# Performance work log

Measured on AMD Instinct MI355X. Metric: run time of the kernel, lower is better.

The kernel has to match this reference:

```python
import jax, jax.numpy as jnp
import numpy as np

N_NODES = 50000
N_EDGES = 800000
IN_DIM = 256
HID = 128
HEADS = 3
N_CLASSES = 40
NEG_SLOPE = 0.2


def gat_conv(x, W, att_src, att_dst, bias, src, dst, n_nodes):
    # x: [N, F_in]; W: [F_in, H*C]; att_*: [H, C]; bias: [H*C]
    H, C = att_src.shape
    h = (x @ W).reshape(n_nodes, H, C)                       # [N,H,C]
    a_src = jnp.einsum('nhc,hc->nh', h, att_src)             # [N,H]
    a_dst = jnp.einsum('nhc,hc->nh', h, att_dst)             # [N,H]
    alpha = jax.nn.leaky_relu(a_src[src] + a_dst[dst], NEG_SLOPE)  # [E,H]
    # softmax over incoming edges per destination node (stable, segment-based)
    amax = jax.ops.segment_max(alpha, dst, num_segments=n_nodes)   # [N,H]
    amax = jnp.where(jnp.isfinite(amax), amax, 0.0)
    ex = jnp.exp(alpha - amax[dst])                          # [E,H]
    denom = jax.ops.segment_sum(ex, dst, num_segments=n_nodes)     # [N,H]
    attn = ex / (denom[dst] + 1e-16)                         # [E,H]
    msg = h[src] * attn[:, :, None]                          # [E,H,C]
    out = jax.ops.segment_sum(msg, dst, num_segments=n_nodes)      # [N,H,C]
    return out.reshape(n_nodes, H * C) + bias


def setup_inputs() -> dict:
    key = jax.random.key(0)
    ks = jax.random.split(key, 12)
    x = jax.random.normal(ks[0], (N_NODES, IN_DIM), dtype=jnp.float32)
    edge_index = jax.random.randint(ks[1], (2, N_EDGES), 0, N_NODES, dtype=jnp.int64)
    s = 0.05
    HC = HEADS * HID
    return {
        'x': x,
        'edge_index': edge_index,
        'W1': jax.random.normal(ks[2], (IN_DIM, HC), dtype=jnp.float32) * s,
        'att_src1': jax.random.normal(ks[3], (HEADS, HID), dtype=jnp.float32) * s,
        'att_dst1': jax.random.normal(ks[4], (HEADS, HID), dtype=jnp.float32) * s,
        'b1': jnp.zeros((HC,), dtype=jnp.float32),
        'W2': jax.random.normal(ks[5], (HC, HC), dtype=jnp.float32) * s,
        'att_src2': jax.random.normal(ks[6], (HEADS, HID), dtype=jnp.float32) * s,
        'att_dst2': jax.random.normal(ks[7], (HEADS, HID), dtype=jnp.float32) * s,
        'b2': jnp.zeros((HC,), dtype=jnp.float32),
        'outW': jax.random.normal(ks[8], (HC, N_CLASSES), dtype=jnp.float32) * s,
        'outb': jnp.zeros((N_CLASSES,), dtype=jnp.float32),
    }


def reference(x, edge_index, W1, att_src1, att_dst1, b1, W2, att_src2, att_dst2, b2, outW, outb):
    n = x.shape[0]
    # PyG GATConv default: add self loops
    loops = jnp.arange(n, dtype=edge_index.dtype)
    src = jnp.concatenate([edge_index[0], loops])
    dst = jnp.concatenate([edge_index[1], loops])
    h = gat_conv(x, W1, att_src1, att_dst1, b1, src, dst, n)
    h = jax.nn.relu(h)  # dropout=0 -> identity
    h = gat_conv(h, W2, att_src2, att_dst2, b2, src, dst, n)
    h = jax.nn.relu(h)
    return h @ outW + outb
```

## Files before the change

kernel.cpp:

```cpp
#include <hip/hip_runtime.h>
#include <cstdint>
#include <cstddef>

typedef unsigned short u16;
typedef unsigned int   u32;
typedef __attribute__((ext_vector_type(8))) short bf16x8;
typedef __attribute__((ext_vector_type(4))) float f32x4;

#define N_NODES 50000
#define N_EDGES 800000
#define ET (N_EDGES + N_NODES)
#define IN_DIM 256
#define HID 128
#define HEADS 3
#define HC 384
#define NCLS 40
#define CAP 96

__device__ __forceinline__ u16 f2bf(float f) {
    union { float f; u32 u; } x; x.f = f;
    u32 r = x.u + 0x7fffu + ((x.u >> 16) & 1u);
    return (u16)(r >> 16);
}
__device__ __forceinline__ float bf2f(u16 b) {
    union { u32 u; float f; } x; x.u = ((u32)b) << 16; return x.f;
}

__device__ __forceinline__ void gload_lds16(const void* g, void* l) {
    __builtin_amdgcn_global_load_lds((const __attribute__((address_space(1))) void*)g,
                                     (__attribute__((address_space(3))) void*)l, 16, 0, 0);
}

__device__ __forceinline__ float rdlane_f(float v, int l) {
    return __int_as_float(__builtin_amdgcn_readlane(__float_as_int(v), l));
}

__global__ __launch_bounds__(256) void count_scatter(const int* __restrict__ ei,
                                                     int* __restrict__ cnt,
                                                     int* __restrict__ bucket)
{
    int e = blockIdx.x * 256 + threadIdx.x;
    if (e >= ET) return;
    int s, d;
    if (e < N_EDGES) { s = ei[e]; d = ei[N_EDGES + e]; }
    else             { s = e - N_EDGES; d = s; }
    int pos = atomicAdd(&cnt[d], 1);
    if (pos < CAP) bucket[d * CAP + pos] = s;
}

__global__ __launch_bounds__(256) void cvt_bf16(const float* __restrict__ in,
                                                u16* __restrict__ o, int n4)
{
    int i = blockIdx.x * 256 + threadIdx.x;
    if (i >= n4) return;
    float4 v = reinterpret_cast<const float4*>(in)[i];
    ushort4 h = { f2bf(v.x), f2bf(v.y), f2bf(v.z), f2bf(v.w) };
    reinterpret_cast<ushort4*>(o)[i] = h;
}

__global__ __launch_bounds__(256) void split_wt(const float* __restrict__ W,
                                                u16* __restrict__ WtH,
                                                u16* __restrict__ WtL, int K)
{
    int idx = blockIdx.x * 256 + threadIdx.x;
    if (idx >= K * HC) return;
    int k = idx / HC, n = idx - k * HC;
    float v = W[idx];
    u16 h = f2bf(v);
    size_t o = ((size_t)(k >> 3) * HC + n) * 8 + (k & 7);
    WtH[o] = h;
    WtL[o] = f2bf(v - bf2f(h));
}

__global__ __launch_bounds__(256) void split_wo(const float* __restrict__ Wo,
                                                u16* __restrict__ WoH,
                                                u16* __restrict__ WoL)
{
    int idx = blockIdx.x * 256 + threadIdx.x;
    if (idx >= HC * 64) return;
    int k = idx >> 6, n = idx & 63;
    float v = (n < NCLS) ? Wo[k * NCLS + n] : 0.f;
    u16 h = f2bf(v);
    size_t o = ((size_t)(k >> 3) * 64 + n) * 8 + (k & 7);
    WoH[o] = h;
    WoL[o] = f2bf(v - bf2f(h));
}

#define BM 128
#define BN 128
#define BK 32
__global__ __launch_bounds__(256) void gemm_mfma(const u16* __restrict__ A,
                                                 const u16* __restrict__ Bh, const u16* __restrict__ Bl,
                                                 u16* __restrict__ Cb, int M, int K)
{
    __shared__ u16 sA0[BM * BK], sA1[BM * BK];
    const int tid = threadIdx.x;
    const int ln  = tid & 63;
    const int wv  = tid >> 6;
    const int bm  = blockIdx.y * BM;
    const int bn  = blockIdx.x * BN;
    const int wm  = (wv >> 1) * 64;
    const int wn  = (wv & 1) * 64;
    const int kg  = ln >> 4;
    const int lr  = ln & 15;
    const int nK  = K >> 5;

    f32x4 acc[4][4] = {};

    auto stage = [&](u16* dA, int ko) {
#pragma unroll
        for (int rnd = 0; rnd < 2; ++rnd) {
            int c   = rnd * 256 + wv * 64 + ln;
            int row = c & 127;
            int kgp = c >> 7;
            int ldsOff = (rnd * 256 + wv * 64) * 8;
            int ar = bm + row; if (ar >= M) ar = M - 1;
            gload_lds16(A + (size_t)ar * K + ko + kgp * 8, dA + ldsOff);
        }
    };

    auto step = [&](const u16* curA, u16* nxtA, int kt, bool pref) {
        const int ko = kt * BK;
        bf16x8 bhf[4], blf[4];
        size_t bb = ((size_t)((ko >> 3) + kg) * HC + bn + wn + lr) * 8;
#pragma unroll
        for (int ni = 0; ni < 4; ++ni) {
            bhf[ni] = *reinterpret_cast<const bf16x8*>(Bh + bb + ni * 128);
            blf[ni] = *reinterpret_cast<const bf16x8*>(Bl + bb + ni * 128);
        }
        if (pref) stage(nxtA, ko + BK);
#pragma unroll
        for (int mi = 0; mi < 4; ++mi) {
            bf16x8 ah = *reinterpret_cast<const bf16x8*>(curA + (kg * 128 + wm + mi * 16 + lr) * 8);
#pragma unroll
            for (int ni = 0; ni < 4; ++ni) {
                acc[mi][ni] = __builtin_amdgcn_mfma_f32_16x16x32_bf16(ah, bhf[ni], acc[mi][ni], 0, 0, 0);
                acc[mi][ni] = __builtin_amdgcn_mfma_f32_16x16x32_bf16(ah, blf[ni], acc[mi][ni], 0, 0, 0);
            }
        }
    };

    stage(sA0, 0);
    for (int kt = 0; kt < nK; kt += 2) {
        __syncthreads();
        step(sA0, sA1, kt, true);
        __syncthreads();
        step(sA1, sA0, kt + 1, kt + 2 < nK);
    }

#pragma unroll
    for (int mi = 0; mi < 4; ++mi) {
#pragma unroll
        for (int i = 0; i < 4; ++i) {
            int r = bm + wm + mi * 16 + kg * 4 + i;
            if (r < M) {
#pragma unroll
                for (int ni = 0; ni < 4; ++ni) {
                    Cb[(size_t)r * HC + bn + wn + ni * 16 + lr] = f2bf(acc[mi][ni][i]);
                }
            }
        }
    }
}

#define OM 256
__global__ __launch_bounds__(256) void out_mfma(const u16* __restrict__ Ah, const u16* __restrict__ Al,
                                                const u16* __restrict__ WoH, const u16* __restrict__ WoL,
                                                const float* __restrict__ b,
                                                float* __restrict__ out)
{
    __shared__ u16 sAh[OM * BK], sAl[OM * BK];
    const int tid = threadIdx.x;
    const int ln  = tid & 63;
    const int wv  = tid >> 6;
    const int bm  = blockIdx.x * OM;
    const int kg  = ln >> 4;
    const int lr  = ln & 15;

    f32x4 acc[4][4] = {};

    for (int kt = 0; kt < HC / BK; ++kt) {
        const int ko = kt * BK;
        __syncthreads();
#pragma unroll
        for (int rnd = 0; rnd < 4; ++rnd) {
            int c   = rnd * 256 + wv * 64 + ln;
            int row = c & 255;
            int kgp = c >> 8;
            int ldsOff = (rnd * 256 + wv * 64) * 8;
            int ar = bm + row; if (ar >= N_NODES) ar = N_NODES - 1;
            size_t off = (size_t)ar * HC + ko + kgp * 8;
            gload_lds16(Ah + off, sAh + ldsOff);
            gload_lds16(Al + off, sAl + ldsOff);
        }
        __syncthreads();

        bf16x8 bhf[4], blf[4];
        size_t bb = ((size_t)((ko >> 3) + kg) * 64 + lr) * 8;
#pragma unroll
        for (int ni = 0; ni < 4; ++ni) {
            bhf[ni] = *reinterpret_cast<const bf16x8*>(WoH + bb + ni * 128);
            blf[ni] = *reinterpret_cast<const bf16x8*>(WoL + bb + ni * 128);
        }
#pragma unroll
        for (int mi = 0; mi < 4; ++mi) {
            int off = (kg * 256 + wv * 64 + mi * 16 + lr) * 8;
            bf16x8 ah = *reinterpret_cast<const bf16x8*>(sAh + off);
            bf16x8 al = *reinterpret_cast<const bf16x8*>(sAl + off);
#pragma unroll
            for (int ni = 0; ni < 4; ++ni) {
                acc[mi][ni] = __builtin_amdgcn_mfma_f32_16x16x32_bf16(ah, bhf[ni], acc[mi][ni], 0, 0, 0);
                acc[mi][ni] = __builtin_amdgcn_mfma_f32_16x16x32_bf16(al, bhf[ni], acc[mi][ni], 0, 0, 0);
                acc[mi][ni] = __builtin_amdgcn_mfma_f32_16x16x32_bf16(ah, blf[ni], acc[mi][ni], 0, 0, 0);
            }
        }
    }

#pragma unroll
    for (int mi = 0; mi < 4; ++mi) {
#pragma unroll
        for (int i = 0; i < 4; ++i) {
            int r = bm + wv * 64 + mi * 16 + kg * 4 + i;
            if (r < N_NODES) {
#pragma unroll
                for (int ni = 0; ni < 4; ++ni) {
                    int col = ni * 16 + lr;
                    if (col < NCLS)
                        out[(size_t)r * NCLS + col] = acc[mi][ni][i] + b[col];
                }
            }
        }
    }
}

__global__ __launch_bounds__(256) void scores_kernel(const u16* __restrict__ h,
                                                     const float* __restrict__ att_s,
                                                     const float* __restrict__ att_d,
                                                     float* __restrict__ asrc,
                                                     float* __restrict__ adst)
{
    int gid = blockIdx.x * 256 + threadIdx.x;
    int wid = gid >> 6;
    int lane = gid & 63;
    if (wid >= N_NODES * HEADS) return;
    int nd = wid / 3;
    int hd = wid - nd * 3;
    const u16* hp = h + (size_t)nd * HC + hd * HID;
    float v0 = bf2f(hp[lane]), v1 = bf2f(hp[lane + 64]);
    float s = v0 * att_s[hd * HID + lane] + v1 * att_s[hd * HID + lane + 64];
    float d = v0 * att_d[hd * HID + lane] + v1 * att_d[hd * HID + lane + 64];
#pragma unroll
    for (int off = 32; off; off >>= 1) {
        s += __shfl_xor(s, off);
        d += __shfl_xor(d, off);
    }
    if (lane == 0) { asrc[wid] = s; adst[wid] = d; }
}

__device__ __forceinline__ float lrelu(float x) { return x > 0.f ? x : 0.2f * x; }

__global__ __launch_bounds__(256) void aggregate_kernel(const u16* __restrict__ h,
                                                        const float* __restrict__ asrc,
                                                        const float* __restrict__ adst,
                                                        const int* __restrict__ cnt,
                                                        const int* __restrict__ bucket,
                                                        const float* __restrict__ bias,
                                                        u16* __restrict__ hOut,
                                                        u16* __restrict__ lOut)
{
    int wv = threadIdx.x >> 6;
    int lane = threadIdx.x & 63;
    int nd = blockIdx.x * 4 + wv;
    if (nd >= N_NODES) return;
    int deg = cnt[nd];
    if (deg > CAP) deg = CAP;
    const int* eb = bucket + nd * CAP;
    float ad0 = adst[nd * 3 + 0], ad1 = adst[nd * 3 + 1], ad2 = adst[nd * 3 + 2];

    bool vA = lane < deg, vB = lane + 64 < deg;
    int sA = vA ? eb[lane] : 0;
    int sB = vB ? eb[lane + 64] : 0;
    float xA0 = -1e30f, xA1 = -1e30f, xA2 = -1e30f;
    float xB0 = -1e30f, xB1 = -1e30f, xB2 = -1e30f;
    if (vA) {
        const float* ap = asrc + (size_t)sA * 3;
        xA0 = lrelu(ap[0] + ad0); xA1 = lrelu(ap[1] + ad1); xA2 = lrelu(ap[2] + ad2);
    }
    if (vB) {
        const float* ap = asrc + (size_t)sB * 3;
        xB0 = lrelu(ap[0] + ad0); xB1 = lrelu(ap[1] + ad1); xB2 = lrelu(ap[2] + ad2);
    }
    float m0 = fmaxf(xA0, xB0), m1 = fmaxf(xA1, xB1), m2 = fmaxf(xA2, xB2);
#pragma unroll
    for (int off = 32; off; off >>= 1) {
        m0 = fmaxf(m0, __shfl_xor(m0, off));
        m1 = fmaxf(m1, __shfl_xor(m1, off));
        m2 = fmaxf(m2, __shfl_xor(m2, off));
    }
    float eA0 = expf(xA0 - m0), eA1 = expf(xA1 - m1), eA2 = expf(xA2 - m2);
    float eB0 = expf(xB0 - m0), eB1 = expf(xB1 - m1), eB2 = expf(xB2 - m2);
    float t0 = eA0 + eB0, t1 = eA1 + eB1, t2 = eA2 + eB2;
#pragma unroll
    for (int off = 32; off; off >>= 1) {
        t0 += __shfl_xor(t0, off);
        t1 += __shfl_xor(t1, off);
        t2 += __shfl_xor(t2, off);
    }
    float r0 = 1.f / (t0 + 1e-16f);
    float r1 = 1.f / (t1 + 1e-16f);
    float r2 = 1.f / (t2 + 1e-16f);
    float wA0 = eA0 * r0, wA1 = eA1 * r1, wA2 = eA2 * r2;
    float wB0 = eB0 * r0, wB1 = eB1 * r1, wB2 = eB2 * r2;

    float a00 = 0.f, a01 = 0.f, a10 = 0.f, a11 = 0.f, a20 = 0.f, a21 = 0.f;
    int d0 = deg < 64 ? deg : 64;
    for (int j = 0; j < d0; ++j) {
        int   s  = __builtin_amdgcn_readlane(sA, j);
        float w0 = rdlane_f(wA0, j);
        float w1 = rdlane_f(wA1, j);
        float w2 = rdlane_f(wA2, j);
        const u16* hp = h + (size_t)s * HC;
        ushort2 h0 = *reinterpret_cast<const ushort2*>(hp + lane * 2);
        ushort2 h1 = *reinterpret_cast<const ushort2*>(hp + 128 + lane * 2);
        ushort2 h2 = *reinterpret_cast<const ushort2*>(hp + 256 + lane * 2);
        a00 += bf2f(h0.x) * w0; a01 += bf2f(h0.y) * w0;
        a10 += bf2f(h1.x) * w1; a11 += bf2f(h1.y) * w1;
        a20 += bf2f(h2.x) * w2; a21 += bf2f(h2.y) * w2;
    }
    for (int j = 64; j < deg; ++j) {
        int   s  = __builtin_amdgcn_readlane(sB, j - 64);
        float w0 = rdlane_f(wB0, j - 64);
        float w1 = rdlane_f(wB1, j - 64);
        float w2 = rdlane_f(wB2, j - 64);
        const u16* hp = h + (size_t)s * HC;
        ushort2 h0 = *reinterpret_cast<const ushort2*>(hp + lane * 2);
        ushort2 h1 = *reinterpret_cast<const ushort2*>(hp + 128 + lane * 2);
        ushort2 h2 = *reinterpret_cast<const ushort2*>(hp + 256 + lane * 2);
        a00 += bf2f(h0.x) * w0; a01 += bf2f(h0.y) * w0;
        a10 += bf2f(h1.x) * w1; a11 += bf2f(h1.y) * w1;
        a20 += bf2f(h2.x) * w2; a21 += bf2f(h2.y) * w2;
    }

    size_t base = (size_t)nd * HC;
    float o[6];
    int   c[3] = { lane * 2, 128 + lane * 2, 256 + lane * 2 };
    o[0] = a00 + bias[c[0]];     o[1] = a01 + bias[c[0] + 1];
    o[2] = a10 + bias[c[1]];     o[3] = a11 + bias[c[1] + 1];
    o[4] = a20 + bias[c[2]];     o[5] = a21 + bias[c[2] + 1];
#pragma unroll
    for (int k = 0; k < 6; ++k) o[k] = o[k] > 0.f ? o[k] : 0.f;
    if (lOut) {
#pragma unroll
        for (int k = 0; k < 3; ++k) {
            u16 hx = f2bf(o[2 * k]), hy = f2bf(o[2 * k + 1]);
            ushort2 hv = { hx, hy };
            ushort2 lv = { f2bf(o[2 * k] - bf2f(hx)), f2bf(o[2 * k + 1] - bf2f(hy)) };
            *reinterpret_cast<ushort2*>(hOut + base + c[k]) = hv;
            *reinterpret_cast<ushort2*>(lOut + base + c[k]) = lv;
        }
    } else {
#pragma unroll
        for (int k = 0; k < 3; ++k) {
            ushort2 hv = { f2bf(o[2 * k]), f2bf(o[2 * k + 1]) };
            *reinterpret_cast<ushort2*>(hOut + base + c[k]) = hv;
        }
    }
}

extern "C" void kernel_launch(void* const* d_in, const int* in_sizes, int n_in,
                              void* d_out, int out_size, void* d_ws, size_t ws_size,
                              hipStream_t stream)
{
    const float* x    = (const float*)d_in[0];
    const int*   ei   = (const int*)d_in[1];
    const float* W1   = (const float*)d_in[2];
    const float* as1  = (const float*)d_in[3];
    const float* ad1  = (const float*)d_in[4];
    const float* b1   = (const float*)d_in[5];
    const float* W2   = (const float*)d_in[6];
    const float* as2  = (const float*)d_in[7];
    const float* ad2  = (const float*)d_in[8];
    const float* b2   = (const float*)d_in[9];
    const float* outW = (const float*)d_in[10];
    const float* outb = (const float*)d_in[11];
    float* out = (float*)d_out;

    u16*   hB   = (u16*)d_ws;
    u16*   aggH = hB + (size_t)N_NODES * HC;
    u16*   aggL = aggH + (size_t)N_NODES * HC;
    u16*   xB   = aggH;
    char*  tail = (char*)(aggL + (size_t)N_NODES * HC);
    u16* W1tH = (u16*)tail;
    u16* W1tL = W1tH + (size_t)IN_DIM * HC;
    u16* W2tH = W1tL + (size_t)IN_DIM * HC;
    u16* W2tL = W2tH + (size_t)HC * HC;
    u16* WoH  = W2tL + (size_t)HC * HC;
    u16* WoL  = WoH + (size_t)HC * 64;
    float* asrc = (float*)(WoL + (size_t)HC * 64);
    float* adst = asrc + (size_t)N_NODES * HEADS;
    int*   cnt    = (int*)(adst + (size_t)N_NODES * HEADS);
    int*   bucket = cnt + N_NODES;

    hipMemsetAsync(cnt, 0, N_NODES * sizeof(int), stream);
    count_scatter<<<(ET + 255) / 256, 256, 0, stream>>>(ei, cnt, bucket);

    cvt_bf16<<<(N_NODES * IN_DIM / 4 + 255) / 256, 256, 0, stream>>>(x, xB, N_NODES * IN_DIM / 4);
    split_wt<<<(IN_DIM * HC + 255) / 256, 256, 0, stream>>>(W1, W1tH, W1tL, IN_DIM);
    split_wt<<<(HC * HC + 255) / 256, 256, 0, stream>>>(W2, W2tH, W2tL, HC);
    split_wo<<<(HC * 64 + 255) / 256, 256, 0, stream>>>(outW, WoH, WoL);

    dim3 gg(HC / BN, (N_NODES + BM - 1) / BM);
    gemm_mfma<<<gg, 256, 0, stream>>>(xB, W1tH, W1tL, hB, N_NODES, IN_DIM);
    scores_kernel<<<(N_NODES * HEADS + 3) / 4, 256, 0, stream>>>(hB, as1, ad1, asrc, adst);
    aggregate_kernel<<<(N_NODES + 3) / 4, 256, 0, stream>>>(hB, asrc, adst, cnt, bucket, b1,
                                                            aggH, nullptr);
    gemm_mfma<<<gg, 256, 0, stream>>>(aggH, W2tH, W2tL, hB, N_NODES, HC);
    scores_kernel<<<(N_NODES * HEADS + 3) / 4, 256, 0, stream>>>(hB, as2, ad2, asrc, adst);
    aggregate_kernel<<<(N_NODES + 3) / 4, 256, 0, stream>>>(hB, asrc, adst, cnt, bucket, b2,
                                                            aggH, aggL);
    out_mfma<<<(N_NODES + OM - 1) / OM, 256, 0, stream>>>(aggH, aggL, WoH, WoL, outb, out);
}
```

Before: 533.5 us.

## Fuse attention score computation into GEMM epilogue and widen aggregate loads

```diff
diff --git a/kernel.cpp b/kernel.cpp
--- a/kernel.cpp
+++ b/kernel.cpp
@@ -91,9 +91,14 @@
 #define BK 32
 __global__ __launch_bounds__(256) void gemm_mfma(const u16* __restrict__ A,
                                                  const u16* __restrict__ Bh, const u16* __restrict__ Bl,
+                                                 const float* __restrict__ att_s,
+                                                 const float* __restrict__ att_d,
+                                                 float* __restrict__ asrc,
+                                                 float* __restrict__ adst,
                                                  u16* __restrict__ Cb, int M, int K)
 {
     __shared__ u16 sA0[BM * BK], sA1[BM * BK];
+    __shared__ float sS[2][BM], sD[2][BM];
     const int tid = threadIdx.x;
     const int ln  = tid & 63;
     const int wv  = tid >> 6;
@@ -161,6 +166,43 @@
             }
         }
     }
+
+    const int hd = blockIdx.x;
+    float as_[4], ad_[4];
+#pragma unroll
+    for (int ni = 0; ni < 4; ++ni) {
+        int colh = wn + ni * 16 + lr;
+        as_[ni] = att_s[hd * HID + colh];
+        ad_[ni] = att_d[hd * HID + colh];
+    }
+#pragma unroll
+    for (int mi = 0; mi < 4; ++mi) {
+#pragma unroll
+        for (int i = 0; i < 4; ++i) {
+            float ps = acc[mi][0][i] * as_[0] + acc[mi][1][i] * as_[1]
+                     + acc[mi][2][i] * as_[2] + acc[mi][3][i] * as_[3];
+            float pd = acc[mi][0][i] * ad_[0] + acc[mi][1][i] * ad_[1]
+                     + acc[mi][2][i] * ad_[2] + acc[mi][3][i] * ad_[3];
+#pragma unroll
+            for (int off = 1; off < 16; off <<= 1) {
+                ps += __shfl_xor(ps, off);
+                pd += __shfl_xor(pd, off);
+            }
+            if (lr == 0) {
+                int rl = wm + mi * 16 + kg * 4 + i;
+                sS[wv & 1][rl] = ps;
+                sD[wv & 1][rl] = pd;
+            }
+        }
+    }
+    __syncthreads();
+    if (tid < BM) {
+        int r = bm + tid;
+        if (r < M) {
+            asrc[r * 3 + hd] = sS[0][tid] + sS[1][tid];
+            adst[r * 3 + hd] = sD[0][tid] + sD[1][tid];
+        }
+    }
 }
 
 #define OM 256
@@ -233,30 +275,6 @@
     }
 }
 
-__global__ __launch_bounds__(256) void scores_kernel(const u16* __restrict__ h,
-                                                     const float* __restrict__ att_s,
-                                                     const float* __restrict__ att_d,
-                                                     float* __restrict__ asrc,
-                                                     float* __restrict__ adst)
-{
-    int gid = blockIdx.x * 256 + threadIdx.x;
-    int wid = gid >> 6;
-    int lane = gid & 63;
-    if (wid >= N_NODES * HEADS) return;
-    int nd = wid / 3;
-    int hd = wid - nd * 3;
-    const u16* hp = h + (size_t)nd * HC + hd * HID;
-    float v0 = bf2f(hp[lane]), v1 = bf2f(hp[lane + 64]);
-    float s = v0 * att_s[hd * HID + lane] + v1 * att_s[hd * HID + lane + 64];
-    float d = v0 * att_d[hd * HID + lane] + v1 * att_d[hd * HID + lane + 64];
-#pragma unroll
-    for (int off = 32; off; off >>= 1) {
-        s += __shfl_xor(s, off);
-        d += __shfl_xor(d, off);
-    }
-    if (lane == 0) { asrc[wid] = s; adst[wid] = d; }
-}
-
 __device__ __forceinline__ float lrelu(float x) { return x > 0.f ? x : 0.2f * x; }
 
 __global__ __launch_bounds__(256) void aggregate_kernel(const u16* __restrict__ h,
@@ -312,58 +330,55 @@
     float wA0 = eA0 * r0, wA1 = eA1 * r1, wA2 = eA2 * r2;
     float wB0 = eB0 * r0, wB1 = eB1 * r1, wB2 = eB2 * r2;
 
-    float a00 = 0.f, a01 = 0.f, a10 = 0.f, a11 = 0.f, a20 = 0.f, a21 = 0.f;
+    float b0 = 0.f, b1 = 0.f, b2 = 0.f, b3 = 0.f, b4 = 0.f, b5 = 0.f;
     int d0 = deg < 64 ? deg : 64;
+#pragma unroll 2
     for (int j = 0; j < d0; ++j) {
         int   s  = __builtin_amdgcn_readlane(sA, j);
         float w0 = rdlane_f(wA0, j);
         float w1 = rdlane_f(wA1, j);
         float w2 = rdlane_f(wA2, j);
+        float wh = lane < 32 ? w0 : w1;
         const u16* hp = h + (size_t)s * HC;
-        ushort2 h0 = *reinterpret_cast<const ushort2*>(hp + lane * 2);
-        ushort2 h1 = *reinterpret_cast<const ushort2*>(hp + 128 + lane * 2);
-        ushort2 h2 = *reinterpret_cast<const ushort2*>(hp + 256 + lane * 2);
-        a00 += bf2f(h0.x) * w0; a01 += bf2f(h0.y) * w0;
-        a10 += bf2f(h1.x) * w1; a11 += bf2f(h1.y) * w1;
-        a20 += bf2f(h2.x) * w2; a21 += bf2f(h2.y) * w2;
+        ushort4 v4 = *reinterpret_cast<const ushort4*>(hp + lane * 4);
+        ushort2 v2 = *reinterpret_cast<const ushort2*>(hp + 256 + lane * 2);
+        b0 += bf2f(v4.x) * wh; b1 += bf2f(v4.y) * wh;
+        b2 += bf2f(v4.z) * wh; b3 += bf2f(v4.w) * wh;
+        b4 += bf2f(v2.x) * w2; b5 += bf2f(v2.y) * w2;
     }
     for (int j = 64; j < deg; ++j) {
         int   s  = __builtin_amdgcn_readlane(sB, j - 64);
         float w0 = rdlane_f(wB0, j - 64);
         float w1 = rdlane_f(wB1, j - 64);
         float w2 = rdlane_f(wB2, j - 64);
+        float wh = lane < 32 ? w0 : w1;
         const u16* hp = h + (size_t)s * HC;
-        ushort2 h0 = *reinterpret_cast<const ushort2*>(hp + lane * 2);
-        ushort2 h1 = *reinterpret_cast<const ushort2*>(hp + 128 + lane * 2);
-        ushort2 h2 = *reinterpret_cast<const ushort2*>(hp + 256 + lane * 2);
-        a00 += bf2f(h0.x) * w0; a01 += bf2f(h0.y) * w0;
-        a10 += bf2f(h1.x) * w1; a11 += bf2f(h1.y) * w1;
-        a20 += bf2f(h2.x) * w2; a21 += bf2f(h2.y) * w2;
+        ushort4 v4 = *reinterpret_cast<const ushort4*>(hp + lane * 4);
+        ushort2 v2 = *reinterpret_cast<const ushort2*>(hp + 256 + lane * 2);
+        b0 += bf2f(v4.x) * wh; b1 += bf2f(v4.y) * wh;
+        b2 += bf2f(v4.z) * wh; b3 += bf2f(v4.w) * wh;
+        b4 += bf2f(v2.x) * w2; b5 += bf2f(v2.y) * w2;
     }
 
     size_t base = (size_t)nd * HC;
-    float o[6];
-    int   c[3] = { lane * 2, 128 + lane * 2, 256 + lane * 2 };
-    o[0] = a00 + bias[c[0]];     o[1] = a01 + bias[c[0] + 1];
-    o[2] = a10 + bias[c[1]];     o[3] = a11 + bias[c[1] + 1];
-    o[4] = a20 + bias[c[2]];     o[5] = a21 + bias[c[2] + 1];
-#pragma unroll
-    for (int k = 0; k < 6; ++k) o[k] = o[k] > 0.f ? o[k] : 0.f;
+    int c4 = lane * 4, c2 = 256 + lane * 2;
+    float4 bb4 = *reinterpret_cast<const float4*>(bias + c4);
+    float2 bb2 = *reinterpret_cast<const float2*>(bias + c2);
+    float o0 = b0 + bb4.x, o1 = b1 + bb4.y, o2 = b2 + bb4.z, o3 = b3 + bb4.w;
+    float o4 = b4 + bb2.x, o5 = b5 + bb2.y;
+    o0 = o0 > 0.f ? o0 : 0.f;  o1 = o1 > 0.f ? o1 : 0.f;
+    o2 = o2 > 0.f ? o2 : 0.f;  o3 = o3 > 0.f ? o3 : 0.f;
+    o4 = o4 > 0.f ? o4 : 0.f;  o5 = o5 > 0.f ? o5 : 0.f;
+    ushort4 hv4 = { f2bf(o0), f2bf(o1), f2bf(o2), f2bf(o3) };
+    ushort2 hv2 = { f2bf(o4), f2bf(o5) };
+    *reinterpret_cast<ushort4*>(hOut + base + c4) = hv4;
+    *reinterpret_cast<ushort2*>(hOut + base + c2) = hv2;
     if (lOut) {
-#pragma unroll
-        for (int k = 0; k < 3; ++k) {
-            u16 hx = f2bf(o[2 * k]), hy = f2bf(o[2 * k + 1]);
-            ushort2 hv = { hx, hy };
-            ushort2 lv = { f2bf(o[2 * k] - bf2f(hx)), f2bf(o[2 * k + 1] - bf2f(hy)) };
-            *reinterpret_cast<ushort2*>(hOut + base + c[k]) = hv;
-            *reinterpret_cast<ushort2*>(lOut + base + c[k]) = lv;
-        }
-    } else {
-#pragma unroll
-        for (int k = 0; k < 3; ++k) {
-            ushort2 hv = { f2bf(o[2 * k]), f2bf(o[2 * k + 1]) };
-            *reinterpret_cast<ushort2*>(hOut + base + c[k]) = hv;
-        }
+        ushort4 lv4 = { f2bf(o0 - bf2f(hv4.x)), f2bf(o1 - bf2f(hv4.y)),
+                        f2bf(o2 - bf2f(hv4.z)), f2bf(o3 - bf2f(hv4.w)) };
+        ushort2 lv2 = { f2bf(o4 - bf2f(hv2.x)), f2bf(o5 - bf2f(hv2.y)) };
+        *reinterpret_cast<ushort4*>(lOut + base + c4) = lv4;
+        *reinterpret_cast<ushort2*>(lOut + base + c2) = lv2;
     }
 }
 
@@ -410,12 +425,10 @@
     split_wo<<<(HC * 64 + 255) / 256, 256, 0, stream>>>(outW, WoH, WoL);
 
     dim3 gg(HC / BN, (N_NODES + BM - 1) / BM);
-    gemm_mfma<<<gg, 256, 0, stream>>>(xB, W1tH, W1tL, hB, N_NODES, IN_DIM);
-    scores_kernel<<<(N_NODES * HEADS + 3) / 4, 256, 0, stream>>>(hB, as1, ad1, asrc, adst);
+    gemm_mfma<<<gg, 256, 0, stream>>>(xB, W1tH, W1tL, as1, ad1, asrc, adst, hB, N_NODES, IN_DIM);
     aggregate_kernel<<<(N_NODES + 3) / 4, 256, 0, stream>>>(hB, asrc, adst, cnt, bucket, b1,
                                                             aggH, nullptr);
-    gemm_mfma<<<gg, 256, 0, stream>>>(aggH, W2tH, W2tL, hB, N_NODES, HC);
-    scores_kernel<<<(N_NODES * HEADS + 3) / 4, 256, 0, stream>>>(hB, as2, ad2, asrc, adst);
+    gemm_mfma<<<gg, 256, 0, stream>>>(aggH, W2tH, W2tL, as2, ad2, asrc, adst, hB, N_NODES, HC);
     aggregate_kernel<<<(N_NODES + 3) / 4, 256, 0, stream>>>(hB, asrc, adst, cnt, bucket, b2,
                                                             aggH, aggL);
     out_mfma<<<(N_NODES + OM - 1) / OM, 256, 0, stream>>>(aggH, aggL, WoH, WoL, outb, out);
```

Result: faster. 505.1 us (-5.3%).
